# Kernel optimization log

Hardware: AMD Instinct MI355X
Metric: run time of the kernel (lower is better)

Reference implementation:

```python
import jax, jax.numpy as jnp
import numpy as np


def setup_inputs() -> dict:
    key = jax.random.key(0)
    k1, k2 = jax.random.split(key)
    N, C, H, W = 8, 19, 384, 384
    logits = jax.random.normal(k1, (N, C, H, W), dtype=jnp.float32)
    label = jax.random.randint(k2, (N, H, W), 0, C).astype(jnp.int64)
    return {"logits": logits, "label": label}


def reference(logits, label):
    # LovaszSoftmaxV1.forward with reduction='mean'.
    # Labels are all valid (none == ignore_index=-100), so the ignore filter
    # is the identity and is omitted for static shapes under jit.
    n, c, h, w = logits.shape
    lg = jnp.transpose(logits, (1, 0, 2, 3)).reshape(c, -1).astype(jnp.float32)  # [C, M]
    lb = label.reshape(-1)                                                        # [M]
    probs = jax.nn.softmax(lg, axis=0)                                            # [C, M]
    one_hot = jax.lax.stop_gradient(
        jax.nn.one_hot(lb, c, dtype=probs.dtype).T)                               # [C, M], detached
    errs = jnp.abs(one_hot - probs)                                               # [C, M]
    # descending sort per class; indices carry no gradient
    order = jax.lax.stop_gradient(jnp.argsort(-errs, axis=1))                     # [C, M]
    errs_sort = jnp.take_along_axis(errs, order, axis=1)
    lb_sort = jnp.take_along_axis(one_hot, order, axis=1)
    # Lovasz extension of the Jaccard loss gradient (computed without grad)
    n_pos = lb_sort.sum(axis=1, keepdims=True)                                    # [C, 1]
    inter = n_pos - jnp.cumsum(lb_sort, axis=1)
    union = n_pos + jnp.cumsum(1.0 - lb_sort, axis=1)
    jacc = 1.0 - inter / union
    jacc = jnp.concatenate([jacc[:, :1], jacc[:, 1:] - jacc[:, :-1]], axis=1)
    jacc = jax.lax.stop_gradient(jacc)
    losses = jnp.einsum('ab,ab->a', errs_sort, jacc)                              # [C]
    return losses.mean(), errs
```

## Files before the change

kernel.cpp:

```cpp
#include <hip/hip_runtime.h>

#define NCLS 19
#define HW   147456
#define MPIX 1179648
#define NB   256
#define TPB  192
#define NBLK 1536
#define HSZ  (NCLS * NB)

typedef float vfloat4 __attribute__((ext_vector_type(4)));

__global__ void __launch_bounds__(TPB) softmax_err_hist(
    const float* __restrict__ logits,
    const int* __restrict__ label,
    float* __restrict__ errs,
    unsigned long long* __restrict__ hist64)
{
    __shared__ unsigned int hist[HSZ];
    const int tid = threadIdx.x;
    const int b = blockIdx.x;

    for (int i = tid; i < HSZ; i += TPB) hist[i] = 0u;
    __syncthreads();

    const int m = (b * TPB + tid) * 4;
    const int n = m / HW;
    const int base = m + n * (NCLS - 1) * HW;

    const int4 lbl = *(const int4*)(label + m);

    float4 mx = make_float4(-1e30f, -1e30f, -1e30f, -1e30f);
    float4 s  = make_float4(0.f, 0.f, 0.f, 0.f);
#pragma unroll
    for (int c = 0; c < NCLS; ++c) {
        float4 x = *(const float4*)(logits + base + c * HW);
        float4 nm;
        nm.x = fmaxf(mx.x, x.x); nm.y = fmaxf(mx.y, x.y);
        nm.z = fmaxf(mx.z, x.z); nm.w = fmaxf(mx.w, x.w);
        s.x = s.x * __expf(mx.x - nm.x) + __expf(x.x - nm.x);
        s.y = s.y * __expf(mx.y - nm.y) + __expf(x.y - nm.y);
        s.z = s.z * __expf(mx.z - nm.z) + __expf(x.z - nm.z);
        s.w = s.w * __expf(mx.w - nm.w) + __expf(x.w - nm.w);
        mx = nm;
    }
    float4 inv = make_float4(1.f / s.x, 1.f / s.y, 1.f / s.z, 1.f / s.w);

#pragma unroll
    for (int c = 0; c < NCLS; ++c) {
        float4 x = *(const float4*)(logits + base + c * HW);
        float4 p;
        p.x = __expf(x.x - mx.x) * inv.x;
        p.y = __expf(x.y - mx.y) * inv.y;
        p.z = __expf(x.z - mx.z) * inv.z;
        p.w = __expf(x.w - mx.w) * inv.w;
        float4 err;
        err.x = (c == lbl.x) ? (1.0f - p.x) : p.x;
        err.y = (c == lbl.y) ? (1.0f - p.y) : p.y;
        err.z = (c == lbl.z) ? (1.0f - p.z) : p.z;
        err.w = (c == lbl.w) ? (1.0f - p.w) : p.w;
        vfloat4 ev; ev.x = err.x; ev.y = err.y; ev.z = err.z; ev.w = err.w;
        __builtin_nontemporal_store(ev, (vfloat4*)(errs + (size_t)c * MPIX + m));

        int k0 = min(max((int)(err.x * (float)NB), 0), NB - 1);
        int k1 = min(max((int)(err.y * (float)NB), 0), NB - 1);
        int k2 = min(max((int)(err.z * (float)NB), 0), NB - 1);
        int k3 = min(max((int)(err.w * (float)NB), 0), NB - 1);
        atomicAdd(&hist[c * NB + k0], 1u + ((c == lbl.x) ? 65536u : 0u));
        atomicAdd(&hist[c * NB + k1], 1u + ((c == lbl.y) ? 65536u : 0u));
        atomicAdd(&hist[c * NB + k2], 1u + ((c == lbl.z) ? 65536u : 0u));
        atomicAdd(&hist[c * NB + k3], 1u + ((c == lbl.w) ? 65536u : 0u));
    }
    __syncthreads();

    for (int i = tid; i < HSZ; i += TPB) {
        unsigned int w = hist[i];
        if (w) {
            unsigned long long add =
                (unsigned long long)(w & 0xFFFFu) |
                ((unsigned long long)(w >> 16) << 32);
            atomicAdd(&hist64[i], add);
        }
    }
}

__device__ __forceinline__ double jaccval(unsigned int n, unsigned int p, unsigned int npos)
{
    unsigned int denom = (npos - p) + n;
    if (denom == 0u) return 0.0;
    return 1.0 - (double)(npos - p) / (double)denom;
}

__global__ void __launch_bounds__(NB) lovasz_scan(
    const unsigned long long* __restrict__ hist64,
    float* __restrict__ out0)
{
    const int c = blockIdx.x;
    const int t = threadIdx.x;

    __shared__ unsigned int cntS[NB], posS[NB];
    unsigned long long w = hist64[c * NB + t];
    cntS[t] = (unsigned int)(w & 0xFFFFFFFFull);
    posS[t] = (unsigned int)(w >> 32);
    __syncthreads();

    unsigned int N = 0, P = 0, totP = 0;
    for (int u = 0; u < NB; ++u) {
        totP += posS[u];
        if (u > t) { N += cntS[u]; P += posS[u]; }
    }

    double Jprev = jaccval(N, P, totP);
    N += cntS[t]; P += posS[t];
    double Jnew = jaccval(N, P, totP);
    double acc = 0.5 * (Jprev + Jnew);

    __shared__ double red[NB];
    red[t] = acc;
    __syncthreads();
    for (int s2 = NB / 2; s2 > 0; s2 >>= 1) {
        if (t < s2) red[t] += red[t + s2];
        __syncthreads();
    }
    if (t == 0) {
        double loss_c = red[0] / (double)NB;
        atomicAdd(out0, (float)(loss_c / (double)NCLS));
    }
}

extern "C" void kernel_launch(void* const* d_in, const int* in_sizes, int n_in,
                              void* d_out, int out_size, void* d_ws, size_t ws_size,
                              hipStream_t stream)
{
    const float* logits = (const float*)d_in[0];
    const int*   label  = (const int*)d_in[1];
    float* out = (float*)d_out;

    unsigned long long* hist64 = (unsigned long long*)d_ws;

    hipMemsetAsync(d_ws, 0, (size_t)HSZ * sizeof(unsigned long long), stream);
    hipMemsetAsync(d_out, 0, sizeof(float), stream);

    softmax_err_hist<<<NBLK, TPB, 0, stream>>>(logits, label, out + 1, hist64);
    lovasz_scan<<<NCLS, NB, 0, stream>>>(hist64, out);
}
```

Before: 230.0 us.

## Keep logits in registers, issue loads before histogram init, use plain stores

Loads all 19 class logits per thread into registers up front, before the shared histogram is cleared, so the global loads overlap the clearing and the logits are read once instead of twice. The softmax becomes a two-pass max-then-exp computed from registers, and the exponentials are reused for the probabilities instead of being recomputed. Nontemporal stores of errs are replaced with ordinary float4 stores, and the launch bounds now request 4 blocks per CU. The trade-off is higher register use (76 floats per thread for the logits), which could limit occupancy or cause spills.

```diff
diff --git a/kernel.cpp b/kernel.cpp
--- a/kernel.cpp
+++ b/kernel.cpp
@@ -8,9 +8,7 @@
 #define NBLK 1536
 #define HSZ  (NCLS * NB)
 
-typedef float vfloat4 __attribute__((ext_vector_type(4)));
-
-__global__ void __launch_bounds__(TPB) softmax_err_hist(
+__global__ void __launch_bounds__(TPB, 4) softmax_err_hist(
     const float* __restrict__ logits,
     const int* __restrict__ label,
     float* __restrict__ errs,
@@ -20,46 +18,47 @@
     const int tid = threadIdx.x;
     const int b = blockIdx.x;
 
-    for (int i = tid; i < HSZ; i += TPB) hist[i] = 0u;
-    __syncthreads();
-
     const int m = (b * TPB + tid) * 4;
     const int n = m / HW;
     const int base = m + n * (NCLS - 1) * HW;
 
     const int4 lbl = *(const int4*)(label + m);
+    float4 v[NCLS];
+#pragma unroll
+    for (int c = 0; c < NCLS; ++c)
+        v[c] = *(const float4*)(logits + base + c * HW);
+
+    for (int i = tid; i < HSZ; i += TPB) hist[i] = 0u;
+    __syncthreads();
 
     float4 mx = make_float4(-1e30f, -1e30f, -1e30f, -1e30f);
-    float4 s  = make_float4(0.f, 0.f, 0.f, 0.f);
 #pragma unroll
     for (int c = 0; c < NCLS; ++c) {
-        float4 x = *(const float4*)(logits + base + c * HW);
-        float4 nm;
-        nm.x = fmaxf(mx.x, x.x); nm.y = fmaxf(mx.y, x.y);
-        nm.z = fmaxf(mx.z, x.z); nm.w = fmaxf(mx.w, x.w);
-        s.x = s.x * __expf(mx.x - nm.x) + __expf(x.x - nm.x);
-        s.y = s.y * __expf(mx.y - nm.y) + __expf(x.y - nm.y);
-        s.z = s.z * __expf(mx.z - nm.z) + __expf(x.z - nm.z);
-        s.w = s.w * __expf(mx.w - nm.w) + __expf(x.w - nm.w);
-        mx = nm;
+        mx.x = fmaxf(mx.x, v[c].x); mx.y = fmaxf(mx.y, v[c].y);
+        mx.z = fmaxf(mx.z, v[c].z); mx.w = fmaxf(mx.w, v[c].w);
+    }
+    float4 s = make_float4(0.f, 0.f, 0.f, 0.f);
+#pragma unroll
+    for (int c = 0; c < NCLS; ++c) {
+        float4 e;
+        e.x = __expf(v[c].x - mx.x); e.y = __expf(v[c].y - mx.y);
+        e.z = __expf(v[c].z - mx.z); e.w = __expf(v[c].w - mx.w);
+        v[c] = e;
+        s.x += e.x; s.y += e.y; s.z += e.z; s.w += e.w;
     }
     float4 inv = make_float4(1.f / s.x, 1.f / s.y, 1.f / s.z, 1.f / s.w);
 
 #pragma unroll
     for (int c = 0; c < NCLS; ++c) {
-        float4 x = *(const float4*)(logits + base + c * HW);
         float4 p;
-        p.x = __expf(x.x - mx.x) * inv.x;
-        p.y = __expf(x.y - mx.y) * inv.y;
-        p.z = __expf(x.z - mx.z) * inv.z;
-        p.w = __expf(x.w - mx.w) * inv.w;
+        p.x = v[c].x * inv.x; p.y = v[c].y * inv.y;
+        p.z = v[c].z * inv.z; p.w = v[c].w * inv.w;
         float4 err;
         err.x = (c == lbl.x) ? (1.0f - p.x) : p.x;
         err.y = (c == lbl.y) ? (1.0f - p.y) : p.y;
         err.z = (c == lbl.z) ? (1.0f - p.z) : p.z;
         err.w = (c == lbl.w) ? (1.0f - p.w) : p.w;
-        vfloat4 ev; ev.x = err.x; ev.y = err.y; ev.z = err.z; ev.w = err.w;
-        __builtin_nontemporal_store(ev, (vfloat4*)(errs + (size_t)c * MPIX + m));
+        *(float4*)(errs + (size_t)c * MPIX + m) = err;
 
         int k0 = min(max((int)(err.x * (float)NB), 0), NB - 1);
         int k1 = min(max((int)(err.y * (float)NB), 0), NB - 1);
```

Result: faster. 216.5 us (-5.9%).
